# Performance work log

Measured on AMD Instinct MI355X. Metric: run time of the kernel, lower is better.

Reference implementation:

```python
import jax, jax.numpy as jnp
import numpy as np

T, M, N = 16, 1024, 10000
N_IN, N_B = 8000, 100


def setup_inputs() -> dict:
    key = jax.random.key(0)
    ks = jax.random.split(key, 7)
    x = jax.random.normal(ks[0], (T, 3, M), dtype=jnp.float32)
    weight = jax.random.normal(ks[1], (N, 4 * M, 2), dtype=jnp.float32) * 0.02
    # 1-based node indices, as the original module subtracts 1
    node_in = jax.random.randint(ks[2], (N_IN,), 1, N + 1)
    top = jax.random.randint(ks[3], (N_B,), 1, N + 1)
    bottom = jax.random.randint(ks[4], (N_B,), 1, N + 1)
    left = jax.random.randint(ks[5], (N_B,), 1, N + 1)
    right = jax.random.randint(ks[6], (N_B,), 1, N + 1)
    return {"x": x, "weight": weight, "node_in": node_in,
            "top": top, "bottom": bottom, "left": left, "right": right}


def reference(x, weight, node_in, top, bottom, left, right):
    t, _, m = x.shape
    # Vectorized form of the nested scatter loop:
    # x_out[i, 4m:4m+4] = [x[i,0,m], x[i,2,m], x[i,2,m], x[i,1,m]]
    x_out = jnp.stack([x[:, 0, :], x[:, 2, :], x[:, 2, :], x[:, 1, :]],
                      axis=-1).reshape(t, 4 * m)  # [T, 4M]
    # torch.matmul([1,T,4M], [N,4M,2]) broadcast -> [N, T, 2]
    f = jnp.einsum('ti,nio->nto', x_out, weight)
    f_in = f[node_in - 1]  # [N_in, T, 2]
    s_top = f[top - 1, :, 1].sum(axis=0)      # [T]
    s_bot = f[bottom - 1, :, 1].sum(axis=0)
    s_left = f[left - 1, :, 0].sum(axis=0)
    s_right = f[right - 1, :, 0].sum(axis=0)
    f_b = jnp.stack([s_top, s_bot, s_left, s_right,
                     s_top + s_bot, s_left + s_right], axis=0)[..., None]  # [6, T, 1]
    return f_in, f_b
```

## Files before the change

### kernel.cpp

```cpp
#include <hip/hip_runtime.h>
#include <stdint.h>

#define T_DIM 16
#define M_DIM 1024
#define N_NODES 10000
#define NB 100
#define N_IN 8000
#define KI 4096
#define KP 8192
#define CHUNKS 16
#define I_CHUNK (KI / CHUNKS)
#define M_CHUNK (I_CHUNK / 4)
#define STEPS ((KP / CHUNKS) / 32)
#define PITCH (I_CHUNK + 4)
#define TILES 625
#define SLAB (N_NODES * T_DIM * 2)

typedef short short8 __attribute__((ext_vector_type(8)));
typedef float f32x4 __attribute__((ext_vector_type(4)));

__device__ __forceinline__ unsigned int fbits(float f) {
    return __builtin_bit_cast(unsigned int, f);
}
__device__ __forceinline__ unsigned int bf16rne(unsigned int u) {
    return (u + 0x7FFFu + ((u >> 16) & 1u)) >> 16;
}
__device__ __forceinline__ unsigned int pack2bf(float a, float b) {
    return bf16rne(fbits(a)) | (bf16rne(fbits(b)) << 16);
}
__device__ __forceinline__ unsigned int cvtpk(float a, float b) {
    unsigned int r;
    asm("v_cvt_pk_bf16_f32 %0, %1, %2" : "=v"(r) : "v"(a), "v"(b));
    return r;
}

__global__ __launch_bounds__(1024) void dedup_kernel(
    const int* __restrict__ node_in,
    const int* __restrict__ top, const int* __restrict__ bottom,
    const int* __restrict__ left, const int* __restrict__ right,
    int* __restrict__ counter, int* __restrict__ list)
{
    __shared__ int flags[N_NODES];
    __shared__ int lcnt;
    const int tid = threadIdx.x;
    for (int i = tid; i < N_NODES; i += 1024) flags[i] = 0;
    if (tid == 0) lcnt = 0;
    __syncthreads();
    for (int i = tid; i < N_IN + 4 * NB; i += 1024) {
        int v;
        if (i < N_IN)              v = node_in[i];
        else if (i < N_IN + NB)    v = top[i - N_IN];
        else if (i < N_IN + 2*NB)  v = bottom[i - N_IN - NB];
        else if (i < N_IN + 3*NB)  v = left[i - N_IN - 2*NB];
        else                       v = right[i - N_IN - 3*NB];
        flags[v - 1] = 1;
    }
    __syncthreads();
    const int lane = tid & 63;
    for (int i = tid; i < N_NODES; i += 1024) {
        int f = flags[i];
        unsigned long long mask = __ballot(f);
        int prefix = __popcll(mask & ((1ull << lane) - 1ull));
        int base = 0;
        if (lane == 0) base = atomicAdd(&lcnt, (int)__popcll(mask));
        base = __shfl(base, 0);
        if (f) list[base + prefix] = i;
    }
    __syncthreads();
    if (tid == 0) *counter = lcnt;
}

__global__ __launch_bounds__(256) void gemm_kernel(
    const float* __restrict__ x,
    const float* __restrict__ weight,
    const int* __restrict__ list,
    const int* __restrict__ counter,
    float* __restrict__ fws)
{
    __shared__ unsigned short lds_x[T_DIM * PITCH];
    __shared__ unsigned short lds_b[4][16 * 256];

    const int tid = threadIdx.x;
    const int chunk = blockIdx.y;

    const int cnt = *counter;
    if (blockIdx.x * 64 >= cnt) return;

    for (int q = tid; q < T_DIM * M_CHUNK; q += 256) {
        int t = q >> 6;
        int mloc = q & 63;
        int m = chunk * M_CHUNK + mloc;
        const float* xb = x + t * 3 * M_DIM + m;
        float v0 = xb[0];
        float v1 = xb[M_DIM];
        float v2 = xb[2 * M_DIM];
        unsigned int w0 = cvtpk(v0, v2);
        unsigned int w1 = cvtpk(v2, v1);
        *(uint2*)&lds_x[t * PITCH + mloc * 4] = make_uint2(w0, w1);
    }
    __syncthreads();

    const int wave = tid >> 6;
    const int lane = tid & 63;
    const int tile = blockIdx.x * 4 + wave;
    if (tile * 16 >= cnt) return;

    const int col = lane & 15;
    const int quad = lane >> 4;
    const int idx = tile * 16 + col;
    const int n = (idx < cnt) ? list[idx] : 0;

    const size_t koff = (size_t)chunk * (KP / CHUNKS);
    const unsigned short* xrow = &lds_x[(lane & 15) * PITCH + quad * 4];
    unsigned short* bb = lds_b[wave];

    f32x4 acc0 = {0.f, 0.f, 0.f, 0.f};
    f32x4 acc1 = {0.f, 0.f, 0.f, 0.f};

    #pragma unroll
    for (int s = 0; s < 2; ++s) {
        #pragma unroll
        for (int nd = 0; nd < 16; ++nd) {
            int nn = __shfl(n, nd);
            const float* src = weight + (size_t)nn * KP + koff + s * 256 + lane * 4;
            f32x4 w4 = *(const f32x4*)src;
            unsigned int u0 = cvtpk(w4[0], w4[1]);
            unsigned int u1 = cvtpk(w4[2], w4[3]);
            *(uint2*)&bb[nd * 256 + lane * 4] = make_uint2(u0, u1);
        }

        #pragma unroll
        for (int gs = 0; gs < 8; ++gs) {
            short8 Bv = *(const short8*)&bb[col * 256 + gs * 32 + quad * 8];

            int S = s * 8 + gs;
            uint2 u = *(const uint2*)(xrow + S * 16);
            union { unsigned int ui[4]; short8 v; } A0u, A1u;
            A0u.ui[0] = u.x & 0xFFFFu;      A0u.ui[1] = u.x >> 16;
            A0u.ui[2] = u.y & 0xFFFFu;      A0u.ui[3] = u.y >> 16;
            A1u.ui[0] = u.x << 16;          A1u.ui[1] = u.x & 0xFFFF0000u;
            A1u.ui[2] = u.y << 16;          A1u.ui[3] = u.y & 0xFFFF0000u;

            acc0 = __builtin_amdgcn_mfma_f32_16x16x32_bf16(A0u.v, Bv, acc0, 0, 0, 0);
            acc1 = __builtin_amdgcn_mfma_f32_16x16x32_bf16(A1u.v, Bv, acc1, 0, 0, 0);
        }
    }

    float* slab = fws + (size_t)chunk * SLAB;
    #pragma unroll
    for (int r = 0; r < 4; ++r) {
        int t = quad * 4 + r;
        *(float2*)&slab[((size_t)n * T_DIM + t) * 2] = make_float2(acc0[r], acc1[r]);
    }
}

__global__ __launch_bounds__(256) void gather_kernel(
    const float* __restrict__ fws,
    const int* __restrict__ node_in,
    const int* __restrict__ top, const int* __restrict__ bottom,
    const int* __restrict__ left, const int* __restrict__ right,
    float* __restrict__ out)
{
    const int tid = threadIdx.x;
    if (blockIdx.x < 250) {
        int e4 = blockIdx.x * 1024 + tid * 4;
        int j = e4 >> 5;
        int rem = e4 & 31;
        size_t base = (size_t)(node_in[j] - 1) * 32 + rem;
        float4 v = {0.f, 0.f, 0.f, 0.f};
        #pragma unroll
        for (int c = 0; c < CHUNKS; ++c) {
            float4 s = *(const float4*)&fws[c * (size_t)SLAB + base];
            v.x += s.x; v.y += s.y; v.z += s.z; v.w += s.w;
        }
        *(float4*)&out[e4] = v;
    } else {
        __shared__ float red[256];
        __shared__ float sums[64];
        const int l = tid >> 6;
        const int t = (tid >> 2) & 15;
        const int p = tid & 3;
        const int* lp = (l == 0) ? top : (l == 1) ? bottom : (l == 2) ? left : right;
        const int osel = (l < 2) ? 1 : 0;
        float s = 0.f;
        for (int idx = p; idx < NB; idx += 4) {
            size_t base = (size_t)(lp[idx] - 1) * 32 + t * 2 + osel;
            #pragma unroll
            for (int c = 0; c < CHUNKS; ++c) s += fws[c * (size_t)SLAB + base];
        }
        red[tid] = s;
        __syncthreads();
        if (p == 0)
            sums[tid >> 2] = red[tid] + red[tid + 1] + red[tid + 2] + red[tid + 3];
        __syncthreads();
        if (tid < 96) {
            int row = tid >> 4;
            int tt = tid & 15;
            float v;
            if (row < 4)       v = sums[row * 16 + tt];
            else if (row == 4) v = sums[0 * 16 + tt] + sums[1 * 16 + tt];
            else               v = sums[2 * 16 + tt] + sums[3 * 16 + tt];
            out[256000 + tid] = v;
        }
    }
}

extern "C" void kernel_launch(void* const* d_in, const int* in_sizes, int n_in,
                              void* d_out, int out_size, void* d_ws, size_t ws_size,
                              hipStream_t stream)
{
    const float* x      = (const float*)d_in[0];
    const float* weight = (const float*)d_in[1];
    const int* node_in = (const int*)d_in[2];
    const int* top     = (const int*)d_in[3];
    const int* bottom  = (const int*)d_in[4];
    const int* left    = (const int*)d_in[5];
    const int* right   = (const int*)d_in[6];

    float* fws  = (float*)d_ws;
    int*   cnt  = (int*)(fws + (size_t)CHUNKS * SLAB);
    int*   list = cnt + 1;
    float* out  = (float*)d_out;

    dedup_kernel<<<1, 1024, 0, stream>>>(node_in, top, bottom, left, right, cnt, list);

    dim3 grid((TILES + 3) / 4, CHUNKS);
    gemm_kernel<<<grid, 256, 0, stream>>>(x, weight, list, cnt, fws);
    gather_kernel<<<251, 256, 0, stream>>>(fws, node_in, top, bottom, left, right, out);
}
```

Measured before the change: 461.4 us.

## Drop dedup pass, compute all nodes densely, and XOR-swizzle LDS B tile

Removes the single-block dedup kernel that built a list of referenced nodes, and instead has the GEMM compute every node contiguously with no index indirection or counter read. This eliminates a serial launch and the gather-by-list loads, but computes all 10000 nodes rather than only the referenced subset (about 5500 unique with random indices). It also adds an XOR swizzle to the per-wave LDS staging of weight rows to reduce bank conflicts on the B-fragment reads.

```diff
diff --git a/kernel.cpp b/kernel.cpp
--- a/kernel.cpp
+++ b/kernel.cpp
@@ -11,7 +11,6 @@
 #define CHUNKS 16
 #define I_CHUNK (KI / CHUNKS)
 #define M_CHUNK (I_CHUNK / 4)
-#define STEPS ((KP / CHUNKS) / 32)
 #define PITCH (I_CHUNK + 4)
 #define TILES 625
 #define SLAB (N_NODES * T_DIM * 2)
@@ -19,62 +18,15 @@
 typedef short short8 __attribute__((ext_vector_type(8)));
 typedef float f32x4 __attribute__((ext_vector_type(4)));
 
-__device__ __forceinline__ unsigned int fbits(float f) {
-    return __builtin_bit_cast(unsigned int, f);
-}
-__device__ __forceinline__ unsigned int bf16rne(unsigned int u) {
-    return (u + 0x7FFFu + ((u >> 16) & 1u)) >> 16;
-}
-__device__ __forceinline__ unsigned int pack2bf(float a, float b) {
-    return bf16rne(fbits(a)) | (bf16rne(fbits(b)) << 16);
-}
 __device__ __forceinline__ unsigned int cvtpk(float a, float b) {
     unsigned int r;
     asm("v_cvt_pk_bf16_f32 %0, %1, %2" : "=v"(r) : "v"(a), "v"(b));
     return r;
 }
 
-__global__ __launch_bounds__(1024) void dedup_kernel(
-    const int* __restrict__ node_in,
-    const int* __restrict__ top, const int* __restrict__ bottom,
-    const int* __restrict__ left, const int* __restrict__ right,
-    int* __restrict__ counter, int* __restrict__ list)
-{
-    __shared__ int flags[N_NODES];
-    __shared__ int lcnt;
-    const int tid = threadIdx.x;
-    for (int i = tid; i < N_NODES; i += 1024) flags[i] = 0;
-    if (tid == 0) lcnt = 0;
-    __syncthreads();
-    for (int i = tid; i < N_IN + 4 * NB; i += 1024) {
-        int v;
-        if (i < N_IN)              v = node_in[i];
-        else if (i < N_IN + NB)    v = top[i - N_IN];
-        else if (i < N_IN + 2*NB)  v = bottom[i - N_IN - NB];
-        else if (i < N_IN + 3*NB)  v = left[i - N_IN - 2*NB];
-        else                       v = right[i - N_IN - 3*NB];
-        flags[v - 1] = 1;
-    }
-    __syncthreads();
-    const int lane = tid & 63;
-    for (int i = tid; i < N_NODES; i += 1024) {
-        int f = flags[i];
-        unsigned long long mask = __ballot(f);
-        int prefix = __popcll(mask & ((1ull << lane) - 1ull));
-        int base = 0;
-        if (lane == 0) base = atomicAdd(&lcnt, (int)__popcll(mask));
-        base = __shfl(base, 0);
-        if (f) list[base + prefix] = i;
-    }
-    __syncthreads();
-    if (tid == 0) *counter = lcnt;
-}
-
 __global__ __launch_bounds__(256) void gemm_kernel(
     const float* __restrict__ x,
     const float* __restrict__ weight,
-    const int* __restrict__ list,
-    const int* __restrict__ counter,
     float* __restrict__ fws)
 {
     __shared__ unsigned short lds_x[T_DIM * PITCH];
@@ -82,9 +34,6 @@
 
     const int tid = threadIdx.x;
     const int chunk = blockIdx.y;
-
-    const int cnt = *counter;
-    if (blockIdx.x * 64 >= cnt) return;
 
     for (int q = tid; q < T_DIM * M_CHUNK; q += 256) {
         int t = q >> 6;
@@ -103,16 +52,15 @@
     const int wave = tid >> 6;
     const int lane = tid & 63;
     const int tile = blockIdx.x * 4 + wave;
-    if (tile * 16 >= cnt) return;
+    if (tile >= TILES) return;
 
     const int col = lane & 15;
     const int quad = lane >> 4;
-    const int idx = tile * 16 + col;
-    const int n = (idx < cnt) ? list[idx] : 0;
+    const int n = tile * 16 + col;
 
     const size_t koff = (size_t)chunk * (KP / CHUNKS);
     const unsigned short* xrow = &lds_x[(lane & 15) * PITCH + quad * 4];
-    unsigned short* bb = lds_b[wave];
+    char* bb = (char*)lds_b[wave];
 
     f32x4 acc0 = {0.f, 0.f, 0.f, 0.f};
     f32x4 acc1 = {0.f, 0.f, 0.f, 0.f};
@@ -121,17 +69,19 @@
     for (int s = 0; s < 2; ++s) {
         #pragma unroll
         for (int nd = 0; nd < 16; ++nd) {
-            int nn = __shfl(n, nd);
-            const float* src = weight + (size_t)nn * KP + koff + s * 256 + lane * 4;
+            const float* src =
+                weight + (size_t)(tile * 16 + nd) * KP + koff + s * 256 + lane * 4;
             f32x4 w4 = *(const f32x4*)src;
             unsigned int u0 = cvtpk(w4[0], w4[1]);
             unsigned int u1 = cvtpk(w4[2], w4[3]);
-            *(uint2*)&bb[nd * 256 + lane * 4] = make_uint2(u0, u1);
+            *(uint2*)(bb + nd * 512 + ((lane * 8) ^ ((nd & 7) << 4))) =
+                make_uint2(u0, u1);
         }
 
         #pragma unroll
         for (int gs = 0; gs < 8; ++gs) {
-            short8 Bv = *(const short8*)&bb[col * 256 + gs * 32 + quad * 8];
+            short8 Bv = *(const short8*)(
+                bb + col * 512 + (((gs * 64 + quad * 16)) ^ ((col & 7) << 4)));
 
             int S = s * 8 + gs;
             uint2 u = *(const uint2*)(xrow + S * 16);
@@ -217,14 +167,10 @@
     const int* left    = (const int*)d_in[5];
     const int* right   = (const int*)d_in[6];
 
-    float* fws  = (float*)d_ws;
-    int*   cnt  = (int*)(fws + (size_t)CHUNKS * SLAB);
-    int*   list = cnt + 1;
-    float* out  = (float*)d_out;
-
-    dedup_kernel<<<1, 1024, 0, stream>>>(node_in, top, bottom, left, right, cnt, list);
+    float* fws = (float*)d_ws;
+    float* out = (float*)d_out;
 
     dim3 grid((TILES + 3) / 4, CHUNKS);
-    gemm_kernel<<<grid, 256, 0, stream>>>(x, weight, list, cnt, fws);
+    gemm_kernel<<<grid, 256, 0, stream>>>(x, weight, fws);
     gather_kernel<<<251, 256, 0, stream>>>(fws, node_in, top, bottom, left, right, out);
 }
```

New measurement: 491.8 us. 6.6% more time.
